# Performance work log

Hardware: AMD Instinct MI355X
Metric: run time of the kernel (lower is better)

The kernel has to match this reference:

```python
import jax, jax.numpy as jnp
import numpy as np
import math

N_NODES = 100000
N_EDGES = 1600000
DIM = 64

def setup_inputs() -> dict:
    key = jax.random.key(0)
    k_x, k_w, k_w1, k_row, k_col, k_dd = jax.random.split(key, 6)
    stdv = 1.0 / math.sqrt(DIM)
    X = jax.random.normal(k_x, (N_NODES, DIM), dtype=jnp.float32)
    W = jax.random.uniform(k_w, (DIM, DIM), dtype=jnp.float32, minval=-stdv, maxval=stdv)
    W1 = jax.random.uniform(k_w1, (DIM, DIM), dtype=jnp.float32, minval=-stdv, maxval=stdv)
    # CSR expansion of the graph: row_ids sorted (destination node of each edge)
    row_ids = jnp.sort(jax.random.randint(k_row, (N_EDGES,), 0, N_NODES, dtype=jnp.int32))
    col_ids = jax.random.randint(k_col, (N_EDGES,), 0, N_NODES, dtype=jnp.int32)
    # degree-like positive normalization vector, bounded away from 0
    dd1 = jax.random.uniform(k_dd, (N_NODES, 1), dtype=jnp.float32, minval=0.5, maxval=1.5)
    return {"X": X, "W": W, "W1": W1, "dd1": dd1, "row_ids": row_ids, "col_ids": col_ids}

def reference(X, W, W1, dd1, row_ids, col_ids):
    # X_prime = X @ W  (dense GEMM)
    XW = X @ W  # [N, D]
    # SpMM aggregation: out[i] = sum_{j in neighbors(i)} XW[j]
    agg = jax.ops.segment_sum(XW[col_ids], row_ids, num_segments=X.shape[0])  # [N, D]
    # per-node normalization + residual branch X @ W1
    return agg / dd1 + X @ W1
```

## Files before the change

### kernel.cpp

```cpp
#include <hip/hip_runtime.h>
#include <hip/hip_bf16.h>

#define DIMS 64
#define BATCH 8

typedef short  bf16x8 __attribute__((ext_vector_type(8)));
typedef float  f32x4v __attribute__((ext_vector_type(4)));
typedef float  f32x2v __attribute__((ext_vector_type(2)));

static __device__ __forceinline__ short f2bf(float f) {
    __hip_bfloat16 h = __float2bfloat16(f);
    return *reinterpret_cast<short*>(&h);
}

__global__ __launch_bounds__(256) void gcn_pre(
    const float* __restrict__ X, const float* __restrict__ W,
    const float* __restrict__ W1, __hip_bfloat16* __restrict__ XWh,
    __hip_bfloat16* __restrict__ XW1h, const int* __restrict__ rows,
    int* __restrict__ ptr, int N, int E, int gemmBlocks)
{
    if (blockIdx.x >= gemmBlocks) {
        const int rb = blockIdx.x - gemmBlocks;
        if (rb == 0 && threadIdx.x < 32)
            reinterpret_cast<uint32_t*>(XWh + ((size_t)N << 6))[threadIdx.x] = 0u;
        const int e = rb * 256 + threadIdx.x;
        if (e >= E) return;
        const int r1 = rows[e];
        const int r0 = (e == 0) ? -1 : rows[e - 1];
        for (int r = r0 + 1; r <= r1; ++r) ptr[r] = e;
        if (e == E - 1) {
            for (int r = r1 + 1; r <= N; ++r) ptr[r] = E;
        }
        return;
    }

    const int w    = threadIdx.x >> 6;
    const int lane = threadIdx.x & 63;
    const int L    = lane & 15;
    const int q    = lane >> 4;

    const int row0 = blockIdx.x * 128 + w * 16;

    bf16x8 bfrag[2][2][4];
    #pragma unroll
    for (int kh = 0; kh < 2; ++kh)
        #pragma unroll
        for (int nt = 0; nt < 4; ++nt)
            #pragma unroll
            for (int j = 0; j < 8; ++j) {
                const int k = kh * 32 + q * 8 + j;
                bfrag[0][kh][nt][j] = f2bf(W [k * 64 + nt * 16 + L]);
                bfrag[1][kh][nt][j] = f2bf(W1[k * 64 + nt * 16 + L]);
            }

    float4 xr[2][2][2];
    #pragma unroll
    for (int t = 0; t < 2; ++t) {
        const int rowA = row0 + t * 64 + L;
        const int rowC = (rowA < N) ? rowA : (N - 1);
        const float* xp = X + (size_t)rowC * 64;
        #pragma unroll
        for (int kh = 0; kh < 2; ++kh) {
            xr[t][kh][0] = reinterpret_cast<const float4*>(xp + kh * 32 + q * 8)[0];
            xr[t][kh][1] = reinterpret_cast<const float4*>(xp + kh * 32 + q * 8)[1];
        }
    }

    #pragma unroll
    for (int t = 0; t < 2; ++t) {
        f32x4v acc[2][4];
        #pragma unroll
        for (int m = 0; m < 2; ++m)
            #pragma unroll
            for (int nt = 0; nt < 4; ++nt)
                acc[m][nt] = (f32x4v){0.f, 0.f, 0.f, 0.f};

        #pragma unroll
        for (int kh = 0; kh < 2; ++kh) {
            const float4 xa = xr[t][kh][0];
            const float4 xb = xr[t][kh][1];
            bf16x8 a;
            a[0] = f2bf(xa.x); a[1] = f2bf(xa.y); a[2] = f2bf(xa.z); a[3] = f2bf(xa.w);
            a[4] = f2bf(xb.x); a[5] = f2bf(xb.y); a[6] = f2bf(xb.z); a[7] = f2bf(xb.w);
            #pragma unroll
            for (int nt = 0; nt < 4; ++nt) {
                acc[0][nt] = __builtin_amdgcn_mfma_f32_16x16x32_bf16(
                    a, bfrag[0][kh][nt], acc[0][nt], 0, 0, 0);
                acc[1][nt] = __builtin_amdgcn_mfma_f32_16x16x32_bf16(
                    a, bfrag[1][kh][nt], acc[1][nt], 0, 0, 0);
            }
        }

        #pragma unroll
        for (int r = 0; r < 4; ++r) {
            const int row = row0 + t * 64 + q * 4 + r;
            if (row < N) {
                ushort4 p0, p1;
                p0.x = (unsigned short)f2bf(acc[0][0][r]);
                p0.y = (unsigned short)f2bf(acc[0][1][r]);
                p0.z = (unsigned short)f2bf(acc[0][2][r]);
                p0.w = (unsigned short)f2bf(acc[0][3][r]);
                p1.x = (unsigned short)f2bf(acc[1][0][r]);
                p1.y = (unsigned short)f2bf(acc[1][1][r]);
                p1.z = (unsigned short)f2bf(acc[1][2][r]);
                p1.w = (unsigned short)f2bf(acc[1][3][r]);
                *reinterpret_cast<ushort4*>(XWh  + ((size_t)row << 6) + 4 * L) = p0;
                *reinterpret_cast<ushort4*>(XW1h + ((size_t)row << 6) + 4 * L) = p1;
            }
        }
    }
}

__global__ __launch_bounds__(256) void gcn_csr(
    const __hip_bfloat16* __restrict__ XWh, const __hip_bfloat16* __restrict__ XW1h,
    const float* __restrict__ dd1, const int* __restrict__ ptr,
    const int* __restrict__ cols, float* __restrict__ out, int N, int E)
{
    const int t    = blockIdx.x * 256 + threadIdx.x;
    const int wave = t >> 6;
    const int lane = threadIdx.x & 63;
    const int g    = lane >> 3;
    const int d    = lane & 7;

    const int row = wave * 8 + g;
    int p0 = 0, p1 = 0;
    float s = 0.f;
    uint4 rr = make_uint4(0u, 0u, 0u, 0u);
    if (row < N) {
        p0 = ptr[row];
        p1 = ptr[row + 1];
        s  = 1.0f / dd1[row];
        rr = *reinterpret_cast<const uint4*>(
            XW1h + (((size_t)row) << 6) + (d << 3));
    }

    f32x2v acc2[4];
    #pragma unroll
    for (int k = 0; k < 4; ++k) acc2[k] = (f32x2v){0.f, 0.f};

    for (int e = p0; __any(e < p1); e += BATCH) {
        uint4 raw[BATCH];
        #pragma unroll
        for (int j = 0; j < BATCH; ++j) {
            const int ee = e + j;
            const int es = (ee < E) ? ee : (E - 1);
            const int cl = cols[es];
            const int c  = (ee < p1) ? cl : N;
            const uint32_t off = ((uint32_t)c << 7) + (uint32_t)(d << 4);
            raw[j] = *reinterpret_cast<const uint4*>(
                reinterpret_cast<const char*>(XWh) + off);
        }
        #pragma unroll
        for (int j = 0; j < BATCH; ++j) {
            const uint32_t ww0 = raw[j].x, ww1 = raw[j].y,
                           ww2 = raw[j].z, ww3 = raw[j].w;
            f32x2v v0, v1, v2, v3;
            v0.x = __uint_as_float(ww0 << 16);
            v0.y = __uint_as_float(ww0 & 0xffff0000u);
            v1.x = __uint_as_float(ww1 << 16);
            v1.y = __uint_as_float(ww1 & 0xffff0000u);
            v2.x = __uint_as_float(ww2 << 16);
            v2.y = __uint_as_float(ww2 & 0xffff0000u);
            v3.x = __uint_as_float(ww3 << 16);
            v3.y = __uint_as_float(ww3 & 0xffff0000u);
            acc2[0] += v0;
            acc2[1] += v1;
            acc2[2] += v2;
            acc2[3] += v3;
        }
    }

    if (row < N) {
        float res[8];
        res[0] = __uint_as_float(rr.x << 16);
        res[1] = __uint_as_float(rr.x & 0xffff0000u);
        res[2] = __uint_as_float(rr.y << 16);
        res[3] = __uint_as_float(rr.y & 0xffff0000u);
        res[4] = __uint_as_float(rr.z << 16);
        res[5] = __uint_as_float(rr.z & 0xffff0000u);
        res[6] = __uint_as_float(rr.w << 16);
        res[7] = __uint_as_float(rr.w & 0xffff0000u);
        const float accs[8] = {acc2[0].x, acc2[0].y, acc2[1].x, acc2[1].y,
                               acc2[2].x, acc2[2].y, acc2[3].x, acc2[3].y};
        #pragma unroll
        for (int tt = 0; tt < 4; ++tt) {
            f32x2v o;
            o.x = accs[tt]     * s + res[tt];
            o.y = accs[4 + tt] * s + res[4 + tt];
            __builtin_nontemporal_store(o, reinterpret_cast<f32x2v*>(
                out + ((size_t)row << 6) + tt * 16 + d * 2));
        }
    }
}

extern "C" void kernel_launch(void* const* d_in, const int* in_sizes, int n_in,
                              void* d_out, int out_size, void* d_ws, size_t ws_size,
                              hipStream_t stream) {
    const float* X   = (const float*)d_in[0];
    const float* W   = (const float*)d_in[1];
    const float* W1  = (const float*)d_in[2];
    const float* dd1 = (const float*)d_in[3];
    const int* rows  = (const int*)d_in[4];
    const int* cols  = (const int*)d_in[5];

    const int N = in_sizes[3];
    const int E = in_sizes[4];

    char* wsp = (char*)d_ws;
    __hip_bfloat16* XWh = (__hip_bfloat16*)wsp;
    size_t off = (((size_t)(N + 1) * DIMS * sizeof(__hip_bfloat16)) + 255) & ~(size_t)255;
    __hip_bfloat16* XW1h = (__hip_bfloat16*)(wsp + off);
    off += (((size_t)N * DIMS * sizeof(__hip_bfloat16)) + 255) & ~(size_t)255;
    int* row_ptr = (int*)(wsp + off);

    float* out = (float*)d_out;

    const int gemmBlocks = (N + 127) / 128;
    const int rptrBlocks = (E + 255) / 256;
    hipLaunchKernelGGL(gcn_pre, dim3(gemmBlocks + rptrBlocks), dim3(256), 0, stream,
                       X, W, W1, XWh, XW1h, rows, row_ptr, N, E, gemmBlocks);

    const int waves  = (N + 7) / 8;
    const int blocks = (waves + 3) / 4;
    hipLaunchKernelGGL(gcn_csr, dim3(blocks), dim3(256), 0, stream,
                       XWh, XW1h, dd1, row_ptr, cols, out, N, E);
}
```

Measured before the change: 128.1 us.

## Stage weight fragments through LDS and prefetch next column-index batch

The GEMM kernel now has each block load W and W1 with coalesced float4 reads, convert them to bf16 and scatter them into shared memory in MFMA fragment order. Each wave then reads its fragments back with vector LDS loads, replacing the strided scalar global loads every thread issued before. The SpMM kernel software-pipelines the column-index loads, fetching the next batch of cols while the current batch's XW gathers are in flight, so the index fetch no longer sits in front of each gather. This costs extra registers for the second index batch and an LDS buffer plus a barrier in the pre kernel.

```diff
diff --git a/kernel.cpp b/kernel.cpp
--- a/kernel.cpp
+++ b/kernel.cpp
@@ -19,6 +19,8 @@
     __hip_bfloat16* __restrict__ XW1h, const int* __restrict__ rows,
     int* __restrict__ ptr, int N, int E, int gemmBlocks)
 {
+    __shared__ short wlds[2 * 2 * 4 * 64 * 8];
+
     if (blockIdx.x >= gemmBlocks) {
         const int rb = blockIdx.x - gemmBlocks;
         if (rb == 0 && threadIdx.x < 32)
@@ -41,17 +43,25 @@
 
     const int row0 = blockIdx.x * 128 + w * 16;
 
-    bf16x8 bfrag[2][2][4];
-    #pragma unroll
-    for (int kh = 0; kh < 2; ++kh)
-        #pragma unroll
-        for (int nt = 0; nt < 4; ++nt)
-            #pragma unroll
-            for (int j = 0; j < 8; ++j) {
-                const int k = kh * 32 + q * 8 + j;
-                bfrag[0][kh][nt][j] = f2bf(W [k * 64 + nt * 16 + L]);
-                bfrag[1][kh][nt][j] = f2bf(W1[k * 64 + nt * 16 + L]);
+    #pragma unroll
+    for (int m = 0; m < 2; ++m) {
+        const float* Wm = m ? W1 : W;
+        #pragma unroll
+        for (int c = 0; c < 4; ++c) {
+            const int f4idx = c * 256 + threadIdx.x;
+            const float4 v = reinterpret_cast<const float4*>(Wm)[f4idx];
+            const float vv[4] = {v.x, v.y, v.z, v.w};
+            #pragma unroll
+            for (int u = 0; u < 4; ++u) {
+                const int i  = f4idx * 4 + u;
+                const int k  = i >> 6, n = i & 63;
+                const int kh = k >> 5, qq = (k >> 3) & 3, j = k & 7;
+                const int nt = n >> 4, LL = n & 15;
+                const int frag = ((m * 2 + kh) * 4 + nt) * 64 + qq * 16 + LL;
+                wlds[frag * 8 + j] = f2bf(vv[u]);
             }
+        }
+    }
 
     float4 xr[2][2][2];
     #pragma unroll
@@ -65,6 +75,18 @@
             xr[t][kh][1] = reinterpret_cast<const float4*>(xp + kh * 32 + q * 8)[1];
         }
     }
+
+    __syncthreads();
+
+    bf16x8 bfrag[2][2][4];
+    #pragma unroll
+    for (int m = 0; m < 2; ++m)
+        #pragma unroll
+        for (int kh = 0; kh < 2; ++kh)
+            #pragma unroll
+            for (int nt = 0; nt < 4; ++nt)
+                bfrag[m][kh][nt] = *reinterpret_cast<const bf16x8*>(
+                    &wlds[(((m * 2 + kh) * 4 + nt) * 64 + lane) * 8]);
 
     #pragma unroll
     for (int t = 0; t < 2; ++t) {
@@ -138,17 +160,32 @@
     #pragma unroll
     for (int k = 0; k < 4; ++k) acc2[k] = (f32x2v){0.f, 0.f};
 
-    for (int e = p0; __any(e < p1); e += BATCH) {
+    int e = p0;
+    int cidx[BATCH];
+    #pragma unroll
+    for (int j = 0; j < BATCH; ++j) {
+        const int ee = e + j;
+        const int es = (ee < E) ? ee : (E - 1);
+        const int cl = cols[es];
+        cidx[j] = (ee < p1) ? cl : N;
+    }
+
+    while (__any(e < p1)) {
         uint4 raw[BATCH];
         #pragma unroll
         for (int j = 0; j < BATCH; ++j) {
-            const int ee = e + j;
+            const uint32_t off = ((uint32_t)cidx[j] << 7) + (uint32_t)(d << 4);
+            raw[j] = *reinterpret_cast<const uint4*>(
+                reinterpret_cast<const char*>(XWh) + off);
+        }
+        const int en = e + BATCH;
+        int cnext[BATCH];
+        #pragma unroll
+        for (int j = 0; j < BATCH; ++j) {
+            const int ee = en + j;
             const int es = (ee < E) ? ee : (E - 1);
             const int cl = cols[es];
-            const int c  = (ee < p1) ? cl : N;
-            const uint32_t off = ((uint32_t)c << 7) + (uint32_t)(d << 4);
-            raw[j] = *reinterpret_cast<const uint4*>(
-                reinterpret_cast<const char*>(XWh) + off);
+            cnext[j] = (ee < p1) ? cl : N;
         }
         #pragma unroll
         for (int j = 0; j < BATCH; ++j) {
@@ -168,6 +205,9 @@
             acc2[2] += v2;
             acc2[3] += v3;
         }
+        #pragma unroll
+        for (int j = 0; j < BATCH; ++j) cidx[j] = cnext[j];
+        e = en;
     }
 
     if (row < N) {
```

Measured after the change: 124.8 us. -2.6%, faster.
